# Kernel optimization log

Measured on AMD Instinct MI355X. Metric: run time of the kernel, lower is better.

## Reference

```python
import jax, jax.numpy as jnp
import numpy as np

GROUP_SIZE = 128
QMAX = 127.0  # int8 symmetric: 2^(8-1) - 1
EPS = 1e-8


def group_quant_dequant(t, group_size=GROUP_SIZE):
    """Group-wise symmetric int8 fake-quantize along the last dim.

    Groups of `group_size` along the last axis share one scale
    s = max|t| / 127; values are rounded/clipped to int8 range and
    immediately dequantized (q * s), which is the exact math of a
    group-quantized GEMM with inline dequantization.
    """
    shape = t.shape
    g = t.reshape(shape[:-1] + (shape[-1] // group_size, group_size))
    s = jnp.maximum(jnp.max(jnp.abs(g), axis=-1, keepdims=True) / QMAX, EPS)
    q = jnp.clip(jnp.round(g / s), -QMAX, QMAX)
    return (q * s).reshape(shape)


def setup_inputs() -> dict:
    key = jax.random.key(0)
    k0, k1, k2, k3 = jax.random.split(key, 4)
    B, S, H, I = 2, 2048, 4096, 11008
    x = jax.random.normal(k0, (B, S, H), dtype=jnp.float32)
    # Linear weights stored [out_features, in_features]; quant groups run
    # along the in_features (contraction) axis.
    w_gate = jax.random.normal(k1, (I, H), dtype=jnp.float32) * (1.0 / np.sqrt(H))
    w_up = jax.random.normal(k2, (I, H), dtype=jnp.float32) * (1.0 / np.sqrt(H))
    w_down = jax.random.normal(k3, (H, I), dtype=jnp.float32) * (1.0 / np.sqrt(I))
    return {"x": x, "w_gate": w_gate, "w_up": w_up, "w_down": w_down}


def reference(x, w_gate, w_up, w_down):
    # quantize input activations (QuantTensor(x))
    xq = group_quant_dequant(x)
    # gate/up quant-GEMMs with inline weight dequant
    gate = jnp.einsum('bsh,ih->bsi', xq, group_quant_dequant(w_gate))
    up = jnp.einsum('bsh,ih->bsi', xq, group_quant_dequant(w_up))
    # SwiGLU: SiLU(gate) * up, then requantize the hidden activation
    hidden = jax.nn.silu(gate) * up
    hq = group_quant_dequant(hidden)
    # down quant-GEMM -> dequantized float output
    out = jnp.einsum('bsi,hi->bsh', hq, group_quant_dequant(w_down))
    return out
```

## Files before the change

### kernel.cpp

```cpp
#include <hip/hip_runtime.h>
#include <math.h>

typedef int i32x4 __attribute__((ext_vector_type(4)));
typedef float f32x4 __attribute__((ext_vector_type(4)));
typedef float f32x2 __attribute__((ext_vector_type(2)));

#define QMAXF 127.0f
#define EPSQ 1e-8f

__device__ __forceinline__ void gl_lds16(const void* g, void* l) {
  __builtin_amdgcn_global_load_lds(
      (const __attribute__((address_space(1))) unsigned int*)g,
      (__attribute__((address_space(3))) unsigned int*)l, 16, 0, 0);
}
__device__ __forceinline__ void gl_lds4(const void* g, void* l) {
  __builtin_amdgcn_global_load_lds(
      (const __attribute__((address_space(1))) unsigned int*)g,
      (__attribute__((address_space(3))) unsigned int*)l, 4, 0, 0);
}

__global__ __launch_bounds__(256)
void qdq8(const float* __restrict__ in, char* __restrict__ q,
          float* __restrict__ sT, long n_groups, int gpr, int R) {
  long grp = (long)blockIdx.x * 8 + (threadIdx.x >> 5);
  if (grp >= n_groups) return;
  int hl = threadIdx.x & 31;
  long base = grp * 128 + hl * 4;
  f32x4 v = *(const f32x4*)(in + base);
  float m = fmaxf(fmaxf(fabsf(v.x), fabsf(v.y)), fmaxf(fabsf(v.z), fabsf(v.w)));
#pragma unroll
  for (int off = 16; off; off >>= 1) m = fmaxf(m, __shfl_xor(m, off));
  float s = fmaxf(m / QMAXF, EPSQ);
  int q0 = (int)fminf(fmaxf(rintf(v.x / s), -QMAXF), QMAXF);
  int q1 = (int)fminf(fmaxf(rintf(v.y / s), -QMAXF), QMAXF);
  int q2 = (int)fminf(fmaxf(rintf(v.z / s), -QMAXF), QMAXF);
  int q3 = (int)fminf(fmaxf(rintf(v.w / s), -QMAXF), QMAXF);
  *(int*)(q + base) = (q0 & 0xff) | ((q1 & 0xff) << 8) |
                      ((q2 & 0xff) << 16) | ((q3 & 0xff) << 24);
  if (hl == 0) {
    long row = grp / gpr;
    long gc = grp - row * gpr;
    sT[gc * (long)R + row] = s;
  }
}


#define GU_SC 131072
#define GU_RMX 135168
#define GU_RS 137216
#define GU_LDS 138240

__global__ __launch_bounds__(512, 2)
void gemm_gu_i8(const char* __restrict__ Aq, const char* __restrict__ Bg,
                const char* __restrict__ Bu,
                const float* __restrict__ sAT, const float* __restrict__ sGT,
                const float* __restrict__ sUT,
                char* __restrict__ Hq, float* __restrict__ sHT,
                int M, int N, int K, int NBN) {
  extern __shared__ __align__(16) char smem[];
  const int tid = threadIdx.x;
  const int lane = tid & 63;
  const int wid = tid >> 6;
  const int wm = wid >> 1, wn = wid & 1;
  const int wr = wm * 64, wc = wn * 64;
  const int l15 = lane & 15, l16 = lane >> 4;

  const int nwg = gridDim.x;
  const int wg = ((int)blockIdx.x & 7) * (nwg >> 3) + ((int)blockIdx.x >> 3);
  const long m0 = (long)(wg / NBN) * 256;
  const long n0 = (long)(wg % NBN) * 128;

  const long rowS = tid >> 3;
  const int offS = ((tid & 7) * 16) ^ ((int)(rowS & 7) << 4);
  const long kstr = 64L * K;
  const char* gA0 = Aq + (m0 + rowS) * K + offS;
  const char* gG0 = Bg + (n0 + rowS) * K + offS;
  const char* gU0 = Bu + (n0 + rowS) * K + offS;

  const int rdSwz = (l15 & 7) << 4;
  const int colK0 = (l16 * 16) ^ rdSwz;
  const int colK1 = (64 + l16 * 16) ^ rdSwz;

  f32x4 accg[4][4], accu[4][4];
#pragma unroll
  for (int i = 0; i < 4; i++)
#pragma unroll
    for (int j = 0; j < 4; j++) {
      accg[i][j] = (f32x4){0.f, 0.f, 0.f, 0.f};
      accu[i][j] = (f32x4){0.f, 0.f, 0.f, 0.f};
    }
  const i32x4 iz = {0, 0, 0, 0};
  const int KG = K >> 7;

#define GU_STAGE(gg, bb)                                                      \
  {                                                                           \
    const long kb = (long)(gg) << 7;                                          \
    char* tb = smem + (bb) * 65536;                                           \
    _Pragma("unroll") for (int k = 0; k < 4; k++)                             \
        gl_lds16(gA0 + kb + k * kstr, tb + (tid + 512 * k) * 16);             \
    _Pragma("unroll") for (int k = 0; k < 2; k++) {                           \
      gl_lds16(gG0 + kb + k * kstr, tb + 32768 + (tid + 512 * k) * 16);       \
      gl_lds16(gU0 + kb + k * kstr, tb + 49152 + (tid + 512 * k) * 16);       \
    }                                                                         \
    char* sc = smem + GU_SC + (bb) * 2048;                                    \
    if (wid < 4) {                                                            \
      gl_lds4(sAT + (long)(gg) * M + m0 + tid, sc + wid * 256);               \
    } else if (wid < 6) {                                                     \
      gl_lds4(sGT + (long)(gg) * N + n0 + (tid - 256), sc + 1024 + (wid - 4) * 256); \
    } else {                                                                  \
      gl_lds4(sUT + (long)(gg) * N + n0 + (tid - 384), sc + 1536 + (wid - 6) * 256); \
    }                                                                         \
  }

  GU_STAGE(0, 0);
  __syncthreads();

  for (int g = 0; g < KG; ++g) {
    const int cb = g & 1;
    if (g + 1 < KG) GU_STAGE(g + 1, cb ^ 1);

    const char* tb = smem + cb * 65536;
    const float* sc = (const float*)(smem + GU_SC + cb * 2048);

    i32x4 af[4][2];
#pragma unroll
    for (int i = 0; i < 4; i++) {
      const int rb = (wr + i * 16 + l15) * 128;
      af[i][0] = *(const i32x4*)(tb + rb + colK0);
      af[i][1] = *(const i32x4*)(tb + rb + colK1);
    }
    f32x4 sa4[4];
#pragma unroll
    for (int i = 0; i < 4; i++)
      sa4[i] = *(const f32x4*)(sc + wr + i * 16 + l16 * 4);

    i32x4 tgP, tuP;
    f32x4 mgP, muP;
#pragma unroll
    for (int j = 0; j < 4; j++) {
      const int rbB = (wc + j * 16 + l15) * 128;
      i32x4 bgf0 = *(const i32x4*)(tb + 32768 + rbB + colK0);
      i32x4 bgf1 = *(const i32x4*)(tb + 32768 + rbB + colK1);
      i32x4 buf0 = *(const i32x4*)(tb + 49152 + rbB + colK0);
      i32x4 buf1 = *(const i32x4*)(tb + 49152 + rbB + colK1);
      float sbg = sc[256 + wc + j * 16 + l15];
      float sbu = sc[384 + wc + j * 16 + l15];
#pragma unroll
      for (int i = 0; i < 4; i++) {
        i32x4 tg = __builtin_amdgcn_mfma_i32_16x16x64_i8(af[i][0], bgf0, iz, 0, 0, 0);
        tg = __builtin_amdgcn_mfma_i32_16x16x64_i8(af[i][1], bgf1, tg, 0, 0, 0);
        i32x4 tu = __builtin_amdgcn_mfma_i32_16x16x64_i8(af[i][0], buf0, iz, 0, 0, 0);
        tu = __builtin_amdgcn_mfma_i32_16x16x64_i8(af[i][1], buf1, tu, 0, 0, 0);
        if (j > 0 || i > 0) {
          const int pf = j * 4 + i - 1;
          const int ip = pf & 3, jp = pf >> 2;
          accg[ip][jp] += mgP * __builtin_convertvector(tgP, f32x4);
          accu[ip][jp] += muP * __builtin_convertvector(tuP, f32x4);
        }
        tgP = tg; tuP = tu;
        mgP = sa4[i] * sbg; muP = sa4[i] * sbu;
      }
    }
    accg[3][3] += mgP * __builtin_convertvector(tgP, f32x4);
    accu[3][3] += muP * __builtin_convertvector(tuP, f32x4);
    __syncthreads();
  }

  float* rmx = (float*)(smem + GU_RMX);
  float* rs = (float*)(smem + GU_RS);
  float pm[4][4];
#pragma unroll
  for (int i = 0; i < 4; i++)
#pragma unroll
    for (int r = 0; r < 4; r++) pm[i][r] = 0.f;
#pragma unroll
  for (int i = 0; i < 4; i++)
#pragma unroll
    for (int j = 0; j < 4; j++)
#pragma unroll
      for (int r = 0; r < 4; r++) {
        float gv = accg[i][j][r];
        float h = gv / (1.f + expf(-gv)) * accu[i][j][r];
        accu[i][j][r] = h;
        pm[i][r] = fmaxf(pm[i][r], fabsf(h));
      }
#pragma unroll
  for (int i = 0; i < 4; i++)
#pragma unroll
    for (int r = 0; r < 4; r++) {
      pm[i][r] = fmaxf(pm[i][r], __shfl_xor(pm[i][r], 1));
      pm[i][r] = fmaxf(pm[i][r], __shfl_xor(pm[i][r], 2));
      pm[i][r] = fmaxf(pm[i][r], __shfl_xor(pm[i][r], 4));
      pm[i][r] = fmaxf(pm[i][r], __shfl_xor(pm[i][r], 8));
    }
#pragma unroll
  for (int i = 0; i < 4; i++)
#pragma unroll
    for (int r = 0; r < 4; r++)
      if (l15 == i * 4 + r) rmx[wn * 256 + wr + i * 16 + l16 * 4 + r] = pm[i][r];
  __syncthreads();
  if (tid < 256) {
    float mx = fmaxf(rmx[tid], rmx[256 + tid]);
    float s = fmaxf(mx / QMAXF, EPSQ);
    rs[tid] = s;
    sHT[(n0 >> 7) * (long)M + m0 + tid] = s;
  }
  __syncthreads();
  char* sQ = smem;
#pragma unroll
  for (int i = 0; i < 4; i++) {
    f32x4 sr = *(const f32x4*)(rs + wr + i * 16 + l16 * 4);
#pragma unroll
    for (int j = 0; j < 4; j++)
#pragma unroll
      for (int r = 0; r < 4; r++) {
        float qv = fminf(fmaxf(rintf(accu[i][j][r] / sr[r]), -QMAXF), QMAXF);
        sQ[(wr + i * 16 + l16 * 4 + r) * 128 + wc + j * 16 + l15] = (char)(int)qv;
      }
  }
  __syncthreads();
  {
    int row = tid >> 1, seg = tid & 1;
    const i32x4* src = (const i32x4*)(sQ + row * 128 + seg * 64);
    i32x4* dst = (i32x4*)(Hq + (m0 + row) * N + n0 + seg * 64);
#pragma unroll
    for (int k = 0; k < 4; k++) dst[k] = src[k];
  }
}

#define DN_SC 98304
#define DN_LDS 101376

__global__ __launch_bounds__(512, 2)
void gemm_dn_i8(const char* __restrict__ Aq, const char* __restrict__ Bq,
                const float* __restrict__ sAT, const float* __restrict__ sBT,
                float* __restrict__ C, int M, int N, int K, int NBN) {
  extern __shared__ __align__(16) char smem[];
  const int tid = threadIdx.x;
  const int lane = tid & 63;
  const int wid = tid >> 6;
  const int wm = wid >> 1, wn = wid & 1;
  const int wr = wm * 64, wc = wn * 64;
  const int l15 = lane & 15, l16 = lane >> 4;

  const int nwg = gridDim.x;
  const int wg = ((int)blockIdx.x & 7) * (nwg >> 3) + ((int)blockIdx.x >> 3);
  const long m0 = (long)(wg / NBN) * 256;
  const long n0 = (long)(wg % NBN) * 128;

  const long rowS = tid >> 3;
  const int offS = ((tid & 7) * 16) ^ ((int)(rowS & 7) << 4);
  const long kstr = 64L * K;
  const char* gA0 = Aq + (m0 + rowS) * K + offS;
  const char* gB0 = Bq + (n0 + rowS) * K + offS;

  const int rdSwz = (l15 & 7) << 4;
  const int colK0 = (l16 * 16) ^ rdSwz;
  const int colK1 = (64 + l16 * 16) ^ rdSwz;

  f32x4 acc[4][4];
#pragma unroll
  for (int i = 0; i < 4; i++)
#pragma unroll
    for (int j = 0; j < 4; j++) acc[i][j] = (f32x4){0.f, 0.f, 0.f, 0.f};
  const i32x4 iz = {0, 0, 0, 0};
  const int KG = K >> 7;

#define DN_STAGE(gg, bb)                                                      \
  {                                                                           \
    const long kb = (long)(gg) << 7;                                          \
    char* tb = smem + (bb) * 49152;                                           \
    _Pragma("unroll") for (int k = 0; k < 4; k++)                             \
        gl_lds16(gA0 + kb + k * kstr, tb + (tid + 512 * k) * 16);             \
    _Pragma("unroll") for (int k = 0; k < 2; k++)                             \
        gl_lds16(gB0 + kb + k * kstr, tb + 32768 + (tid + 512 * k) * 16);     \
    char* sc = smem + DN_SC + (bb) * 1536;                                    \
    if (wid < 4) {                                                            \
      gl_lds4(sAT + (long)(gg) * M + m0 + tid, sc + wid * 256);               \
    } else if (wid < 6) {                                                     \
      gl_lds4(sBT + (long)(gg) * N + n0 + (tid - 256), sc + 1024 + (wid - 4) * 256); \
    }                                                                         \
  }

  DN_STAGE(0, 0);
  __syncthreads();

  for (int g = 0; g < KG; ++g) {
    const int cb = g & 1;
    if (g + 1 < KG) DN_STAGE(g + 1, cb ^ 1);

    const char* tb = smem + cb * 49152;
    const float* sc = (const float*)(smem + DN_SC + cb * 1536);

    i32x4 af[4][2];
#pragma unroll
    for (int i = 0; i < 4; i++) {
      const int rb = (wr + i * 16 + l15) * 128;
      af[i][0] = *(const i32x4*)(tb + rb + colK0);
      af[i][1] = *(const i32x4*)(tb + rb + colK1);
    }
    f32x4 sa4[4];
#pragma unroll
    for (int i = 0; i < 4; i++)
      sa4[i] = *(const f32x4*)(sc + wr + i * 16 + l16 * 4);

    i32x4 tP;
    f32x4 msP;
#pragma unroll
    for (int j = 0; j < 4; j++) {
      const int rbB = (wc + j * 16 + l15) * 128;
      i32x4 bf0 = *(const i32x4*)(tb + 32768 + rbB + colK0);
      i32x4 bf1 = *(const i32x4*)(tb + 32768 + rbB + colK1);
      float sb = sc[256 + wc + j * 16 + l15];
#pragma unroll
      for (int i = 0; i < 4; i++) {
        i32x4 t = __builtin_amdgcn_mfma_i32_16x16x64_i8(af[i][0], bf0, iz, 0, 0, 0);
        t = __builtin_amdgcn_mfma_i32_16x16x64_i8(af[i][1], bf1, t, 0, 0, 0);
        if (j > 0 || i > 0) {
          const int pf = j * 4 + i - 1;
          const int ip = pf & 3, jp = pf >> 2;
          acc[ip][jp] += msP * __builtin_convertvector(tP, f32x4);
        }
        tP = t;
        msP = sa4[i] * sb;
      }
    }
    acc[3][3] += msP * __builtin_convertvector(tP, f32x4);
    __syncthreads();
  }

#pragma unroll
  for (int i = 0; i < 4; i++)
#pragma unroll
    for (int j = 0; j < 4; j++)
#pragma unroll
      for (int r = 0; r < 4; r++) {
        long row = m0 + wr + i * 16 + l16 * 4 + r;
        long col = n0 + wc + j * 16 + l15;
        C[row * N + col] = acc[i][j][r];
      }
}

extern "C" void kernel_launch(void* const* d_in, const int* in_sizes, int n_in,
                              void* d_out, int out_size, void* d_ws, size_t ws_size,
                              hipStream_t stream) {
  (void)n_in; (void)out_size;
  const float* x  = (const float*)d_in[0];
  const float* wg = (const float*)d_in[1];
  const float* wu = (const float*)d_in[2];
  const float* wd = (const float*)d_in[3];
  float* out = (float*)d_out;

  const long H = 4096;
  const long M = in_sizes[0] / H;
  const long I = in_sizes[1] / H;
  const long GH = H >> 7;
  const long GI = I >> 7;

  char* ws = (char*)d_ws;
  size_t off = 0;
  char* xq  = ws + off; off += (size_t)(M * H);
  char* wgq = ws + off; off += (size_t)(I * H);
  char* wuq = ws + off; off += (size_t)(I * H);
  char* wdq = ws + off; off += (size_t)(H * I);
  char* hq  = ws + off; off += (size_t)(M * I);
  float* s_x = (float*)(ws + off); off += (size_t)(GH * M) * 4;
  float* s_g = (float*)(ws + off); off += (size_t)(GH * I) * 4;
  float* s_u = (float*)(ws + off); off += (size_t)(GH * I) * 4;
  float* s_d = (float*)(ws + off); off += (size_t)(GI * H) * 4;
  float* s_h = (float*)(ws + off); off += (size_t)(GI * M) * 4;
  if (ws_size < off) return;

  hipFuncSetAttribute((const void*)gemm_gu_i8,
                      hipFuncAttributeMaxDynamicSharedMemorySize, GU_LDS);
  hipFuncSetAttribute((const void*)gemm_dn_i8,
                      hipFuncAttributeMaxDynamicSharedMemorySize, DN_LDS);

  {
    long ng;
    ng = M * H / 128;
    qdq8<<<dim3((unsigned)((ng + 7) / 8)), dim3(256), 0, stream>>>(x, xq, s_x, ng, (int)GH, (int)M);
    ng = I * H / 128;
    qdq8<<<dim3((unsigned)((ng + 7) / 8)), dim3(256), 0, stream>>>(wg, wgq, s_g, ng, (int)GH, (int)I);
    qdq8<<<dim3((unsigned)((ng + 7) / 8)), dim3(256), 0, stream>>>(wu, wuq, s_u, ng, (int)GH, (int)I);
    ng = H * I / 128;
    qdq8<<<dim3((unsigned)((ng + 7) / 8)), dim3(256), 0, stream>>>(wd, wdq, s_d, ng, (int)GI, (int)H);
  }

  {
    const int NBN = (int)GI;
    const int grid = (int)(M / 256) * NBN;
    gemm_gu_i8<<<dim3(grid), dim3(512), GU_LDS, stream>>>(
        xq, wgq, wuq, s_x, s_g, s_u, hq, s_h, (int)M, (int)I, (int)H, NBN);
  }
  {
    const int NBN = (int)GH;
    const int grid = (int)(M / 256) * NBN;
    gemm_dn_i8<<<dim3(grid), dim3(512), DN_LDS, stream>>>(
        hq, wdq, s_h, s_d, out, (int)M, (int)H, (int)I, NBN);
  }
}
```

Before: 1.062 ms.

## Split gate/up across warp groups with smaller tile and single-buffered LDS

```diff
diff --git a/kernel.cpp b/kernel.cpp
--- a/kernel.cpp
+++ b/kernel.cpp
@@ -45,12 +45,12 @@
 }
 
 
-#define GU_SC 131072
-#define GU_RMX 135168
-#define GU_RS 137216
-#define GU_LDS 138240
-
-__global__ __launch_bounds__(512, 2)
+#define GU_SC 65536
+#define GU_RMX 67072
+#define GU_RS 68096
+#define GU_LDS 68608
+
+__global__ __launch_bounds__(512, 4)
 void gemm_gu_i8(const char* __restrict__ Aq, const char* __restrict__ Bg,
                 const char* __restrict__ Bu,
                 const float* __restrict__ sAT, const float* __restrict__ sGT,
@@ -61,13 +61,14 @@
   const int tid = threadIdx.x;
   const int lane = tid & 63;
   const int wid = tid >> 6;
-  const int wm = wid >> 1, wn = wid & 1;
-  const int wr = wm * 64, wc = wn * 64;
+  const int dw = wid & 3;
+  const bool is_up = wid >= 4;
+  const int wr = (dw >> 1) * 64, wc = (dw & 1) * 64;
   const int l15 = lane & 15, l16 = lane >> 4;
 
   const int nwg = gridDim.x;
   const int wg = ((int)blockIdx.x & 7) * (nwg >> 3) + ((int)blockIdx.x >> 3);
-  const long m0 = (long)(wg / NBN) * 256;
+  const long m0 = (long)(wg / NBN) * 128;
   const long n0 = (long)(wg % NBN) * 128;
 
   const long rowS = tid >> 3;
@@ -81,150 +82,142 @@
   const int colK0 = (l16 * 16) ^ rdSwz;
   const int colK1 = (64 + l16 * 16) ^ rdSwz;
 
-  f32x4 accg[4][4], accu[4][4];
+  f32x4 acc[4][4];
 #pragma unroll
   for (int i = 0; i < 4; i++)
 #pragma unroll
-    for (int j = 0; j < 4; j++) {
-      accg[i][j] = (f32x4){0.f, 0.f, 0.f, 0.f};
-      accu[i][j] = (f32x4){0.f, 0.f, 0.f, 0.f};
-    }
+    for (int j = 0; j < 4; j++) acc[i][j] = (f32x4){0.f, 0.f, 0.f, 0.f};
   const i32x4 iz = {0, 0, 0, 0};
   const int KG = K >> 7;
 
-#define GU_STAGE(gg, bb)                                                      \
-  {                                                                           \
-    const long kb = (long)(gg) << 7;                                          \
-    char* tb = smem + (bb) * 65536;                                           \
-    _Pragma("unroll") for (int k = 0; k < 4; k++)                             \
-        gl_lds16(gA0 + kb + k * kstr, tb + (tid + 512 * k) * 16);             \
-    _Pragma("unroll") for (int k = 0; k < 2; k++) {                           \
-      gl_lds16(gG0 + kb + k * kstr, tb + 32768 + (tid + 512 * k) * 16);       \
-      gl_lds16(gU0 + kb + k * kstr, tb + 49152 + (tid + 512 * k) * 16);       \
-    }                                                                         \
-    char* sc = smem + GU_SC + (bb) * 2048;                                    \
-    if (wid < 4) {                                                            \
-      gl_lds4(sAT + (long)(gg) * M + m0 + tid, sc + wid * 256);               \
-    } else if (wid < 6) {                                                     \
-      gl_lds4(sGT + (long)(gg) * N + n0 + (tid - 256), sc + 1024 + (wid - 4) * 256); \
-    } else {                                                                  \
-      gl_lds4(sUT + (long)(gg) * N + n0 + (tid - 384), sc + 1536 + (wid - 6) * 256); \
-    }                                                                         \
-  }
-
-  GU_STAGE(0, 0);
-  __syncthreads();
-
   for (int g = 0; g < KG; ++g) {
-    const int cb = g & 1;
-    if (g + 1 < KG) GU_STAGE(g + 1, cb ^ 1);
-
-    const char* tb = smem + cb * 65536;
-    const float* sc = (const float*)(smem + GU_SC + cb * 2048);
-
-    i32x4 af[4][2];
-#pragma unroll
-    for (int i = 0; i < 4; i++) {
-      const int rb = (wr + i * 16 + l15) * 128;
-      af[i][0] = *(const i32x4*)(tb + rb + colK0);
-      af[i][1] = *(const i32x4*)(tb + rb + colK1);
+    const long kb = (long)g << 7;
+    gl_lds16(gA0 + kb, smem + tid * 16);
+    gl_lds16(gA0 + kb + kstr, smem + (tid + 512) * 16);
+    gl_lds16(gG0 + kb, smem + 16384 + tid * 16);
+    gl_lds16(gG0 + kb + kstr, smem + 16384 + (tid + 512) * 16);
+    gl_lds16(gU0 + kb, smem + 32768 + tid * 16);
+    gl_lds16(gU0 + kb + kstr, smem + 32768 + (tid + 512) * 16);
+    char* sc8 = smem + GU_SC;
+    if (wid == 0)      gl_lds4(sAT + (long)g * M + m0 + lane,      sc8);
+    else if (wid == 1) gl_lds4(sAT + (long)g * M + m0 + 64 + lane, sc8 + 256);
+    else if (wid == 2) gl_lds4(sGT + (long)g * N + n0 + lane,      sc8 + 512);
+    else if (wid == 3) gl_lds4(sGT + (long)g * N + n0 + 64 + lane, sc8 + 768);
+    else if (wid == 4) gl_lds4(sUT + (long)g * N + n0 + lane,      sc8 + 1024);
+    else if (wid == 5) gl_lds4(sUT + (long)g * N + n0 + 64 + lane, sc8 + 1280);
+    __syncthreads();
+
+    const char* tbB = smem + (is_up ? 32768 : 16384);
+    const float* sc = (const float*)(smem + GU_SC);
+    const float* scB = sc + (is_up ? 256 : 128);
+
+#pragma unroll
+    for (int h = 0; h < 2; ++h) {
+      i32x4 af[2][2];
+      f32x4 sa4[2];
+#pragma unroll
+      for (int ii = 0; ii < 2; ii++) {
+        const int i = h * 2 + ii;
+        const int rb = (wr + i * 16 + l15) * 128;
+        af[ii][0] = *(const i32x4*)(smem + rb + colK0);
+        af[ii][1] = *(const i32x4*)(smem + rb + colK1);
+        sa4[ii] = *(const f32x4*)(sc + wr + i * 16 + l16 * 4);
+      }
+#pragma unroll
+      for (int j = 0; j < 4; j++) {
+        const int rbB = (wc + j * 16 + l15) * 128;
+        i32x4 bf0 = *(const i32x4*)(tbB + rbB + colK0);
+        i32x4 bf1 = *(const i32x4*)(tbB + rbB + colK1);
+        float sb = scB[wc + j * 16 + l15];
+#pragma unroll
+        for (int ii = 0; ii < 2; ii++) {
+          i32x4 t = __builtin_amdgcn_mfma_i32_16x16x64_i8(af[ii][0], bf0, iz, 0, 0, 0);
+          t = __builtin_amdgcn_mfma_i32_16x16x64_i8(af[ii][1], bf1, t, 0, 0, 0);
+          acc[h * 2 + ii][j] += (sa4[ii] * sb) * __builtin_convertvector(t, f32x4);
+        }
+      }
     }
-    f32x4 sa4[4];
-#pragma unroll
-    for (int i = 0; i < 4; i++)
-      sa4[i] = *(const f32x4*)(sc + wr + i * 16 + l16 * 4);
-
-    i32x4 tgP, tuP;
-    f32x4 mgP, muP;
-#pragma unroll
-    for (int j = 0; j < 4; j++) {
-      const int rbB = (wc + j * 16 + l15) * 128;
-      i32x4 bgf0 = *(const i32x4*)(tb + 32768 + rbB + colK0);
-      i32x4 bgf1 = *(const i32x4*)(tb + 32768 + rbB + colK1);
-      i32x4 buf0 = *(const i32x4*)(tb + 49152 + rbB + colK0);
-      i32x4 buf1 = *(const i32x4*)(tb + 49152 + rbB + colK1);
-      float sbg = sc[256 + wc + j * 16 + l15];
-      float sbu = sc[384 + wc + j * 16 + l15];
-#pragma unroll
-      for (int i = 0; i < 4; i++) {
-        i32x4 tg = __builtin_amdgcn_mfma_i32_16x16x64_i8(af[i][0], bgf0, iz, 0, 0, 0);
-        tg = __builtin_amdgcn_mfma_i32_16x16x64_i8(af[i][1], bgf1, tg, 0, 0, 0);
-        i32x4 tu = __builtin_amdgcn_mfma_i32_16x16x64_i8(af[i][0], buf0, iz, 0, 0, 0);
-        tu = __builtin_amdgcn_mfma_i32_16x16x64_i8(af[i][1], buf1, tu, 0, 0, 0);
-        if (j > 0 || i > 0) {
-          const int pf = j * 4 + i - 1;
-          const int ip = pf & 3, jp = pf >> 2;
-          accg[ip][jp] += mgP * __builtin_convertvector(tgP, f32x4);
-          accu[ip][jp] += muP * __builtin_convertvector(tuP, f32x4);
-        }
-        tgP = tg; tuP = tu;
-        mgP = sa4[i] * sbg; muP = sa4[i] * sbu;
-      }
-    }
-    accg[3][3] += mgP * __builtin_convertvector(tgP, f32x4);
-    accu[3][3] += muP * __builtin_convertvector(tuP, f32x4);
     __syncthreads();
   }
 
+  float* gexch = (float*)smem;
+  if (!is_up) {
+#pragma unroll
+    for (int i = 0; i < 4; i++)
+#pragma unroll
+      for (int j = 0; j < 4; j++)
+#pragma unroll
+        for (int r = 0; r < 4; r++)
+          gexch[(wr + i * 16 + l16 * 4 + r) * 128 + wc + j * 16 + l15] = acc[i][j][r];
+  }
+  __syncthreads();
   float* rmx = (float*)(smem + GU_RMX);
   float* rs = (float*)(smem + GU_RS);
-  float pm[4][4];
-#pragma unroll
-  for (int i = 0; i < 4; i++)
-#pragma unroll
-    for (int r = 0; r < 4; r++) pm[i][r] = 0.f;
-#pragma unroll
-  for (int i = 0; i < 4; i++)
-#pragma unroll
-    for (int j = 0; j < 4; j++)
+  if (is_up) {
+    float pm[4][4];
+#pragma unroll
+    for (int i = 0; i < 4; i++)
+#pragma unroll
+      for (int r = 0; r < 4; r++) pm[i][r] = 0.f;
+#pragma unroll
+    for (int i = 0; i < 4; i++)
+#pragma unroll
+      for (int j = 0; j < 4; j++)
+#pragma unroll
+        for (int r = 0; r < 4; r++) {
+          int row = wr + i * 16 + l16 * 4 + r;
+          int col = wc + j * 16 + l15;
+          float gv = gexch[row * 128 + col];
+          float h = gv / (1.f + expf(-gv)) * acc[i][j][r];
+          acc[i][j][r] = h;
+          pm[i][r] = fmaxf(pm[i][r], fabsf(h));
+        }
+#pragma unroll
+    for (int i = 0; i < 4; i++)
 #pragma unroll
       for (int r = 0; r < 4; r++) {
-        float gv = accg[i][j][r];
-        float h = gv / (1.f + expf(-gv)) * accu[i][j][r];
-        accu[i][j][r] = h;
-        pm[i][r] = fmaxf(pm[i][r], fabsf(h));
-      }
-#pragma unroll
-  for (int i = 0; i < 4; i++)
-#pragma unroll
-    for (int r = 0; r < 4; r++) {
-      pm[i][r] = fmaxf(pm[i][r], __shfl_xor(pm[i][r], 1));
-      pm[i][r] = fmaxf(pm[i][r], __shfl_xor(pm[i][r], 2));
-      pm[i][r] = fmaxf(pm[i][r], __shfl_xor(pm[i][r], 4));
-      pm[i][r] = fmaxf(pm[i][r], __shfl_xor(pm[i][r], 8));
-    }
-#pragma unroll
-  for (int i = 0; i < 4; i++)
-#pragma unroll
-    for (int r = 0; r < 4; r++)
-      if (l15 == i * 4 + r) rmx[wn * 256 + wr + i * 16 + l16 * 4 + r] = pm[i][r];
-  __syncthreads();
-  if (tid < 256) {
-    float mx = fmaxf(rmx[tid], rmx[256 + tid]);
+        pm[i][r] = fmaxf(pm[i][r], __shfl_xor(pm[i][r], 1));
+        pm[i][r] = fmaxf(pm[i][r], __shfl_xor(pm[i][r], 2));
+        pm[i][r] = fmaxf(pm[i][r], __shfl_xor(pm[i][r], 4));
+        pm[i][r] = fmaxf(pm[i][r], __shfl_xor(pm[i][r], 8));
+      }
+#pragma unroll
+    for (int i = 0; i < 4; i++)
+#pragma unroll
+      for (int r = 0; r < 4; r++)
+        if (l15 == i * 4 + r)
+          rmx[(dw & 1) * 128 + wr + i * 16 + l16 * 4 + r] = pm[i][r];
+  }
+  __syncthreads();
+  if (tid < 128) {
+    float mx = fmaxf(rmx[tid], rmx[128 + tid]);
     float s = fmaxf(mx / QMAXF, EPSQ);
     rs[tid] = s;
     sHT[(n0 >> 7) * (long)M + m0 + tid] = s;
   }
   __syncthreads();
-  char* sQ = smem;
-#pragma unroll
-  for (int i = 0; i < 4; i++) {
-    f32x4 sr = *(const f32x4*)(rs + wr + i * 16 + l16 * 4);
-#pragma unroll
-    for (int j = 0; j < 4; j++)
-#pragma unroll
-      for (int r = 0; r < 4; r++) {
-        float qv = fminf(fmaxf(rintf(accu[i][j][r] / sr[r]), -QMAXF), QMAXF);
-        sQ[(wr + i * 16 + l16 * 4 + r) * 128 + wc + j * 16 + l15] = (char)(int)qv;
-      }
+  char* qb = smem;
+  if (is_up) {
+#pragma unroll
+    for (int i = 0; i < 4; i++) {
+      f32x4 sr = *(const f32x4*)(rs + wr + i * 16 + l16 * 4);
+#pragma unroll
+      for (int j = 0; j < 4; j++)
+#pragma unroll
+        for (int r = 0; r < 4; r++) {
+          float qv = fminf(fmaxf(rintf(acc[i][j][r] / sr[r]), -QMAXF), QMAXF);
+          qb[(wr + i * 16 + l16 * 4 + r) * 128 + wc + j * 16 + l15] = (char)(int)qv;
+        }
+    }
   }
   __syncthreads();
   {
-    int row = tid >> 1, seg = tid & 1;
-    const i32x4* src = (const i32x4*)(sQ + row * 128 + seg * 64);
-    i32x4* dst = (i32x4*)(Hq + (m0 + row) * N + n0 + seg * 64);
-#pragma unroll
-    for (int k = 0; k < 4; k++) dst[k] = src[k];
+    long row = tid >> 2;
+    int off = (tid & 3) * 32;
+    const i32x4* src = (const i32x4*)(qb + row * 128 + off);
+    i32x4* dst = (i32x4*)(Hq + (m0 + row) * N + n0 + off);
+    dst[0] = src[0];
+    dst[1] = src[1];
   }
 }
 
@@ -389,7 +382,7 @@
 
   {
     const int NBN = (int)GI;
-    const int grid = (int)(M / 256) * NBN;
+    const int grid = (int)(M / 128) * NBN;
     gemm_gu_i8<<<dim3(grid), dim3(512), GU_LDS, stream>>>(
         xq, wgq, wuq, s_x, s_g, s_u, hq, s_h, (int)M, (int)I, (int)H, NBN);
   }
```

Result: slower. 2.024 ms (+90.6%).

## Split fused gate/up GEMM into two single-B GEMMs with fp32 gate spill

Applied to the files above, without the earlier changes.

```diff
diff --git a/kernel.cpp b/kernel.cpp
--- a/kernel.cpp
+++ b/kernel.cpp
@@ -45,196 +45,18 @@
 }
 
 
-#define GU_SC 131072
-#define GU_RMX 135168
-#define GU_RS 137216
-#define GU_LDS 138240
-
+#define DN_SC 98304
+#define DN_RMX 101376
+#define DN_RS 103424
+#define DN_LDS 104448
+
+template<int EPI>
 __global__ __launch_bounds__(512, 2)
-void gemm_gu_i8(const char* __restrict__ Aq, const char* __restrict__ Bg,
-                const char* __restrict__ Bu,
-                const float* __restrict__ sAT, const float* __restrict__ sGT,
-                const float* __restrict__ sUT,
-                char* __restrict__ Hq, float* __restrict__ sHT,
-                int M, int N, int K, int NBN) {
-  extern __shared__ __align__(16) char smem[];
-  const int tid = threadIdx.x;
-  const int lane = tid & 63;
-  const int wid = tid >> 6;
-  const int wm = wid >> 1, wn = wid & 1;
-  const int wr = wm * 64, wc = wn * 64;
-  const int l15 = lane & 15, l16 = lane >> 4;
-
-  const int nwg = gridDim.x;
-  const int wg = ((int)blockIdx.x & 7) * (nwg >> 3) + ((int)blockIdx.x >> 3);
-  const long m0 = (long)(wg / NBN) * 256;
-  const long n0 = (long)(wg % NBN) * 128;
-
-  const long rowS = tid >> 3;
-  const int offS = ((tid & 7) * 16) ^ ((int)(rowS & 7) << 4);
-  const long kstr = 64L * K;
-  const char* gA0 = Aq + (m0 + rowS) * K + offS;
-  const char* gG0 = Bg + (n0 + rowS) * K + offS;
-  const char* gU0 = Bu + (n0 + rowS) * K + offS;
-
-  const int rdSwz = (l15 & 7) << 4;
-  const int colK0 = (l16 * 16) ^ rdSwz;
-  const int colK1 = (64 + l16 * 16) ^ rdSwz;
-
-  f32x4 accg[4][4], accu[4][4];
-#pragma unroll
-  for (int i = 0; i < 4; i++)
-#pragma unroll
-    for (int j = 0; j < 4; j++) {
-      accg[i][j] = (f32x4){0.f, 0.f, 0.f, 0.f};
-      accu[i][j] = (f32x4){0.f, 0.f, 0.f, 0.f};
-    }
-  const i32x4 iz = {0, 0, 0, 0};
-  const int KG = K >> 7;
-
-#define GU_STAGE(gg, bb)                                                      \
-  {                                                                           \
-    const long kb = (long)(gg) << 7;                                          \
-    char* tb = smem + (bb) * 65536;                                           \
-    _Pragma("unroll") for (int k = 0; k < 4; k++)                             \
-        gl_lds16(gA0 + kb + k * kstr, tb + (tid + 512 * k) * 16);             \
-    _Pragma("unroll") for (int k = 0; k < 2; k++) {                           \
-      gl_lds16(gG0 + kb + k * kstr, tb + 32768 + (tid + 512 * k) * 16);       \
-      gl_lds16(gU0 + kb + k * kstr, tb + 49152 + (tid + 512 * k) * 16);       \
-    }                                                                         \
-    char* sc = smem + GU_SC + (bb) * 2048;                                    \
-    if (wid < 4) {                                                            \
-      gl_lds4(sAT + (long)(gg) * M + m0 + tid, sc + wid * 256);               \
-    } else if (wid < 6) {                                                     \
-      gl_lds4(sGT + (long)(gg) * N + n0 + (tid - 256), sc + 1024 + (wid - 4) * 256); \
-    } else {                                                                  \
-      gl_lds4(sUT + (long)(gg) * N + n0 + (tid - 384), sc + 1536 + (wid - 6) * 256); \
-    }                                                                         \
-  }
-
-  GU_STAGE(0, 0);
-  __syncthreads();
-
-  for (int g = 0; g < KG; ++g) {
-    const int cb = g & 1;
-    if (g + 1 < KG) GU_STAGE(g + 1, cb ^ 1);
-
-    const char* tb = smem + cb * 65536;
-    const float* sc = (const float*)(smem + GU_SC + cb * 2048);
-
-    i32x4 af[4][2];
-#pragma unroll
-    for (int i = 0; i < 4; i++) {
-      const int rb = (wr + i * 16 + l15) * 128;
-      af[i][0] = *(const i32x4*)(tb + rb + colK0);
-      af[i][1] = *(const i32x4*)(tb + rb + colK1);
-    }
-    f32x4 sa4[4];
-#pragma unroll
-    for (int i = 0; i < 4; i++)
-      sa4[i] = *(const f32x4*)(sc + wr + i * 16 + l16 * 4);
-
-    i32x4 tgP, tuP;
-    f32x4 mgP, muP;
-#pragma unroll
-    for (int j = 0; j < 4; j++) {
-      const int rbB = (wc + j * 16 + l15) * 128;
-      i32x4 bgf0 = *(const i32x4*)(tb + 32768 + rbB + colK0);
-      i32x4 bgf1 = *(const i32x4*)(tb + 32768 + rbB + colK1);
-      i32x4 buf0 = *(const i32x4*)(tb + 49152 + rbB + colK0);
-      i32x4 buf1 = *(const i32x4*)(tb + 49152 + rbB + colK1);
-      float sbg = sc[256 + wc + j * 16 + l15];
-      float sbu = sc[384 + wc + j * 16 + l15];
-#pragma unroll
-      for (int i = 0; i < 4; i++) {
-        i32x4 tg = __builtin_amdgcn_mfma_i32_16x16x64_i8(af[i][0], bgf0, iz, 0, 0, 0);
-        tg = __builtin_amdgcn_mfma_i32_16x16x64_i8(af[i][1], bgf1, tg, 0, 0, 0);
-        i32x4 tu = __builtin_amdgcn_mfma_i32_16x16x64_i8(af[i][0], buf0, iz, 0, 0, 0);
-        tu = __builtin_amdgcn_mfma_i32_16x16x64_i8(af[i][1], buf1, tu, 0, 0, 0);
-        if (j > 0 || i > 0) {
-          const int pf = j * 4 + i - 1;
-          const int ip = pf & 3, jp = pf >> 2;
-          accg[ip][jp] += mgP * __builtin_convertvector(tgP, f32x4);
-          accu[ip][jp] += muP * __builtin_convertvector(tuP, f32x4);
-        }
-        tgP = tg; tuP = tu;
-        mgP = sa4[i] * sbg; muP = sa4[i] * sbu;
-      }
-    }
-    accg[3][3] += mgP * __builtin_convertvector(tgP, f32x4);
-    accu[3][3] += muP * __builtin_convertvector(tuP, f32x4);
-    __syncthreads();
-  }
-
-  float* rmx = (float*)(smem + GU_RMX);
-  float* rs = (float*)(smem + GU_RS);
-  float pm[4][4];
-#pragma unroll
-  for (int i = 0; i < 4; i++)
-#pragma unroll
-    for (int r = 0; r < 4; r++) pm[i][r] = 0.f;
-#pragma unroll
-  for (int i = 0; i < 4; i++)
-#pragma unroll
-    for (int j = 0; j < 4; j++)
-#pragma unroll
-      for (int r = 0; r < 4; r++) {
-        float gv = accg[i][j][r];
-        float h = gv / (1.f + expf(-gv)) * accu[i][j][r];
-        accu[i][j][r] = h;
-        pm[i][r] = fmaxf(pm[i][r], fabsf(h));
-      }
-#pragma unroll
-  for (int i = 0; i < 4; i++)
-#pragma unroll
-    for (int r = 0; r < 4; r++) {
-      pm[i][r] = fmaxf(pm[i][r], __shfl_xor(pm[i][r], 1));
-      pm[i][r] = fmaxf(pm[i][r], __shfl_xor(pm[i][r], 2));
-      pm[i][r] = fmaxf(pm[i][r], __shfl_xor(pm[i][r], 4));
-      pm[i][r] = fmaxf(pm[i][r], __shfl_xor(pm[i][r], 8));
-    }
-#pragma unroll
-  for (int i = 0; i < 4; i++)
-#pragma unroll
-    for (int r = 0; r < 4; r++)
-      if (l15 == i * 4 + r) rmx[wn * 256 + wr + i * 16 + l16 * 4 + r] = pm[i][r];
-  __syncthreads();
-  if (tid < 256) {
-    float mx = fmaxf(rmx[tid], rmx[256 + tid]);
-    float s = fmaxf(mx / QMAXF, EPSQ);
-    rs[tid] = s;
-    sHT[(n0 >> 7) * (long)M + m0 + tid] = s;
-  }
-  __syncthreads();
-  char* sQ = smem;
-#pragma unroll
-  for (int i = 0; i < 4; i++) {
-    f32x4 sr = *(const f32x4*)(rs + wr + i * 16 + l16 * 4);
-#pragma unroll
-    for (int j = 0; j < 4; j++)
-#pragma unroll
-      for (int r = 0; r < 4; r++) {
-        float qv = fminf(fmaxf(rintf(accu[i][j][r] / sr[r]), -QMAXF), QMAXF);
-        sQ[(wr + i * 16 + l16 * 4 + r) * 128 + wc + j * 16 + l15] = (char)(int)qv;
-      }
-  }
-  __syncthreads();
-  {
-    int row = tid >> 1, seg = tid & 1;
-    const i32x4* src = (const i32x4*)(sQ + row * 128 + seg * 64);
-    i32x4* dst = (i32x4*)(Hq + (m0 + row) * N + n0 + seg * 64);
-#pragma unroll
-    for (int k = 0; k < 4; k++) dst[k] = src[k];
-  }
-}
-
-#define DN_SC 98304
-#define DN_LDS 101376
-
-__global__ __launch_bounds__(512, 2)
-void gemm_dn_i8(const char* __restrict__ Aq, const char* __restrict__ Bq,
-                const float* __restrict__ sAT, const float* __restrict__ sBT,
-                float* __restrict__ C, int M, int N, int K, int NBN) {
+void gemm_i8(const char* __restrict__ Aq, const char* __restrict__ Bq,
+             const float* __restrict__ sAT, const float* __restrict__ sBT,
+             float* __restrict__ C, const float* __restrict__ Gate,
+             char* __restrict__ Hq, float* __restrict__ sHT,
+             int M, int N, int K, int NBN) {
   extern __shared__ __align__(16) char smem[];
   const int tid = threadIdx.x;
   const int lane = tid & 63;
@@ -329,16 +151,81 @@
     __syncthreads();
   }
 
-#pragma unroll
-  for (int i = 0; i < 4; i++)
-#pragma unroll
-    for (int j = 0; j < 4; j++)
+  if (EPI == 0) {
+#pragma unroll
+    for (int i = 0; i < 4; i++)
+#pragma unroll
+      for (int j = 0; j < 4; j++)
+#pragma unroll
+        for (int r = 0; r < 4; r++) {
+          long row = m0 + wr + i * 16 + l16 * 4 + r;
+          long col = n0 + wc + j * 16 + l15;
+          C[row * N + col] = acc[i][j][r];
+        }
+  } else {
+    float* rmx = (float*)(smem + DN_RMX);
+    float* rs = (float*)(smem + DN_RS);
+    float pm[4][4];
+#pragma unroll
+    for (int i = 0; i < 4; i++)
+#pragma unroll
+      for (int r = 0; r < 4; r++) pm[i][r] = 0.f;
+#pragma unroll
+    for (int i = 0; i < 4; i++)
+#pragma unroll
+      for (int j = 0; j < 4; j++)
+#pragma unroll
+        for (int r = 0; r < 4; r++) {
+          long row = m0 + wr + i * 16 + l16 * 4 + r;
+          long col = n0 + wc + j * 16 + l15;
+          float gv = Gate[row * N + col];
+          float h = gv / (1.f + expf(-gv)) * acc[i][j][r];
+          acc[i][j][r] = h;
+          pm[i][r] = fmaxf(pm[i][r], fabsf(h));
+        }
+#pragma unroll
+    for (int i = 0; i < 4; i++)
 #pragma unroll
       for (int r = 0; r < 4; r++) {
-        long row = m0 + wr + i * 16 + l16 * 4 + r;
-        long col = n0 + wc + j * 16 + l15;
-        C[row * N + col] = acc[i][j][r];
+        pm[i][r] = fmaxf(pm[i][r], __shfl_xor(pm[i][r], 1));
+        pm[i][r] = fmaxf(pm[i][r], __shfl_xor(pm[i][r], 2));
+        pm[i][r] = fmaxf(pm[i][r], __shfl_xor(pm[i][r], 4));
+        pm[i][r] = fmaxf(pm[i][r], __shfl_xor(pm[i][r], 8));
       }
+#pragma unroll
+    for (int i = 0; i < 4; i++)
+#pragma unroll
+      for (int r = 0; r < 4; r++)
+        if (l15 == i * 4 + r) rmx[wn * 256 + wr + i * 16 + l16 * 4 + r] = pm[i][r];
+    __syncthreads();
+    if (tid < 256) {
+      float mx = fmaxf(rmx[tid], rmx[256 + tid]);
+      float s = fmaxf(mx / QMAXF, EPSQ);
+      rs[tid] = s;
+      sHT[(n0 >> 7) * (long)M + m0 + tid] = s;
+    }
+    __syncthreads();
+    char* sQ = smem;
+#pragma unroll
+    for (int i = 0; i < 4; i++) {
+      f32x4 sr = *(const f32x4*)(rs + wr + i * 16 + l16 * 4);
+#pragma unroll
+      for (int j = 0; j < 4; j++)
+#pragma unroll
+        for (int r = 0; r < 4; r++) {
+          float qv = fminf(fmaxf(rintf(acc[i][j][r] / sr[r]), -QMAXF), QMAXF);
+          sQ[(wr + i * 16 + l16 * 4 + r) * 128 + wc + j * 16 + l15] = (char)(int)qv;
+        }
+    }
+    __syncthreads();
+    {
+      int row = tid >> 1, seg = tid & 1;
+      const i32x4* src = (const i32x4*)(sQ + row * 128 + seg * 64);
+      i32x4* dst = (i32x4*)(Hq + (m0 + row) * N + n0 + seg * 64);
+#pragma unroll
+      for (int k = 0; k < 4; k++) dst[k] = src[k];
+    }
+  }
 }
 
 extern "C" void kernel_launch(void* const* d_in, const int* in_sizes, int n_in,
@@ -369,11 +256,14 @@
   float* s_u = (float*)(ws + off); off += (size_t)(GH * I) * 4;
   float* s_d = (float*)(ws + off); off += (size_t)(GI * H) * 4;
   float* s_h = (float*)(ws + off); off += (size_t)(GI * M) * 4;
+  float* gate = (float*)(ws + off); off += (size_t)(M * I) * 4;
   if (ws_size < off) return;
 
-  hipFuncSetAttribute((const void*)gemm_gu_i8,
-                      hipFuncAttributeMaxDynamicSharedMemorySize, GU_LDS);
-  hipFuncSetAttribute((const void*)gemm_dn_i8,
+  auto kEpi0 = gemm_i8<0>;
+  auto kEpi1 = gemm_i8<1>;
+  hipFuncSetAttribute((const void*)kEpi0,
+                      hipFuncAttributeMaxDynamicSharedMemorySize, DN_LDS);
+  hipFuncSetAttribute((const void*)kEpi1,
                       hipFuncAttributeMaxDynamicSharedMemorySize, DN_LDS);
 
   {
@@ -390,13 +280,18 @@
   {
     const int NBN = (int)GI;
     const int grid = (int)(M / 256) * NBN;
-    gemm_gu_i8<<<dim3(grid), dim3(512), GU_LDS, stream>>>(
-        xq, wgq, wuq, s_x, s_g, s_u, hq, s_h, (int)M, (int)I, (int)H, NBN);
+    kEpi0<<<dim3(grid), dim3(512), DN_LDS, stream>>>(
+        xq, wgq, s_x, s_g, gate, nullptr, nullptr, nullptr,
+        (int)M, (int)I, (int)H, NBN);
+    kEpi1<<<dim3(grid), dim3(512), DN_LDS, stream>>>(
+        xq, wuq, s_x, s_u, nullptr, gate, hq, s_h,
+        (int)M, (int)I, (int)H, NBN);
   }
   {
     const int NBN = (int)GH;
     const int grid = (int)(M / 256) * NBN;
-    gemm_dn_i8<<<dim3(grid), dim3(512), DN_LDS, stream>>>(
-        hq, wdq, s_h, s_d, out, (int)M, (int)H, (int)I, NBN);
-  }
-}
+    kEpi0<<<dim3(grid), dim3(512), DN_LDS, stream>>>(
+        hq, wdq, s_h, s_d, out, nullptr, nullptr, nullptr,
+        (int)M, (int)H, (int)I, NBN);
+  }
+}
```

After: 1.171 ms. 1.1x slower.
